# Optimization experiments

Measured on AMD Instinct MI355X. Metric: run time of the kernel, lower is better.

## Reference

```python
import jax, jax.numpy as jnp
import numpy as np

N_HEAD = 16
HEAD_SIZE = 64  # n_embd // n_head = 1024 // 16


def setup_inputs() -> dict:
    key = jax.random.key(0)
    k1, k2 = jax.random.split(key)
    B, T, C = 2, 2048, 1024
    x = jax.random.normal(k1, (B, T, C), dtype=jnp.float32)
    w_attn = jax.random.normal(k2, (C, 3 * C), dtype=jnp.float32) * (C ** -0.5)
    b_attn = jnp.zeros((3 * C,), dtype=jnp.float32)
    return {"x": x, "w_attn": w_attn, "b_attn": b_attn}


def reference(x, w_attn, b_attn):
    B, T, C = x.shape
    qkv = x @ w_attn + b_attn  # [B, T, 3C]
    q, k, v = jnp.split(qkv, 3, axis=-1)
    # [B, T, H, D] -> [B, H, T, D]
    def heads(t):
        return t.reshape(B, T, N_HEAD, HEAD_SIZE).transpose(0, 2, 1, 3)
    q, k, v = heads(q), heads(k), heads(v)
    scale = HEAD_SIZE ** -0.5
    wei = jnp.einsum('bhqd,bhkd->bhqk', q, k) * scale  # [B, H, T, T]
    causal = jnp.tril(jnp.ones((T, T), dtype=bool))
    wei = jnp.where(causal, wei, -jnp.inf)
    wei = jax.nn.softmax(wei, axis=-1)
    out = jnp.einsum('bhqk,bhkd->bhqd', wei, v)  # [B, H, T, D]
    out = out.transpose(0, 2, 1, 3).reshape(B, T, C)
    return out
```

## Files before the change

kernel.cpp:

```cpp
#include <hip/hip_runtime.h>
#include <hip/hip_bf16.h>

#define BSZ 2
#define SEQ 2048
#define CDIM 1024
#define NHEAD 16
#define HDIM 64
#define M_GEMM (BSZ * SEQ)
#define N_GEMM (3 * CDIM)
#define K_GEMM CDIM
#define QK_PITCH (2 * CDIM)

typedef __attribute__((ext_vector_type(8))) short short8;
typedef __attribute__((ext_vector_type(4))) short short4v;
typedef __attribute__((ext_vector_type(4))) float f32x4;

__device__ __forceinline__ short bf16_rn(float f) {
    unsigned u = __builtin_bit_cast(unsigned, f);
    u += 0x7FFF + ((u >> 16) & 1);
    return (short)(u >> 16);
}

__device__ __forceinline__ void gl2lds16(const short* g, short* l) {
    __builtin_amdgcn_global_load_lds(
        (const __attribute__((address_space(1))) unsigned int*)g,
        (__attribute__((address_space(3))) unsigned int*)l, 16, 0, 0);
}

#define WAITV4() asm volatile("s_waitcnt vmcnt(4)")
#define WAITV0() asm volatile("s_waitcnt vmcnt(0)")
#define LGKM0()  asm volatile("s_waitcnt lgkmcnt(0)")
#define SCB()    __builtin_amdgcn_sched_barrier(0)
#define BARRIER() __builtin_amdgcn_s_barrier()

__global__ __launch_bounds__(256) void cvt_fused(const float* __restrict__ X,
                                                 const float* __restrict__ W,
                                                 short* __restrict__ Xb,
                                                 short* __restrict__ WT) {
    const int tid = threadIdx.x;
    if (blockIdx.x < 2048) {
        size_t idx = ((size_t)blockIdx.x * 256 + tid) * 8;
        float4 a = *(const float4*)&X[idx];
        float4 b = *(const float4*)&X[idx + 4];
        short8 o;
        o[0] = bf16_rn(a.x); o[1] = bf16_rn(a.y); o[2] = bf16_rn(a.z); o[3] = bf16_rn(a.w);
        o[4] = bf16_rn(b.x); o[5] = bf16_rn(b.y); o[6] = bf16_rn(b.z); o[7] = bf16_rn(b.w);
        *(short8*)&Xb[idx] = o;
        return;
    }
    __shared__ short T[64][72];
    const int bid = blockIdx.x - 2048;
    const int n0 = (bid % 48) * 64;
    const int k0 = (bid / 48) * 64;
#pragma unroll
    for (int pass = 0; pass < 4; ++pass) {
        int i = pass * 256 + tid;
        int kr = i >> 4;
        int n4 = i & 15;
        float4 v = *(const float4*)&W[(size_t)(k0 + kr) * N_GEMM + n0 + n4 * 4];
        T[n4 * 4 + 0][kr] = bf16_rn(v.x);
        T[n4 * 4 + 1][kr] = bf16_rn(v.y);
        T[n4 * 4 + 2][kr] = bf16_rn(v.z);
        T[n4 * 4 + 3][kr] = bf16_rn(v.w);
    }
    __syncthreads();
#pragma unroll
    for (int pass = 0; pass < 2; ++pass) {
        int o = pass * 256 + tid;
        int nr = o >> 3;
        int c8 = o & 7;
        *(short8*)&WT[(size_t)(n0 + nr) * K_GEMM + k0 + c8 * 8] =
            *(const short8*)&T[nr][c8 * 8];
    }
}

#define MFMA_QUAD(MB, NB)                                                     \
    do {                                                                      \
        __builtin_amdgcn_s_setprio(1);                                        \
        _Pragma("unroll")                                                     \
        for (int mi_ = 0; mi_ < 4; ++mi_)                                     \
            _Pragma("unroll")                                                 \
            for (int ni_ = 0; ni_ < 2; ++ni_)                                 \
                _Pragma("unroll")                                             \
                for (int ks_ = 0; ks_ < 2; ++ks_)                             \
                    acc[(MB) + mi_][(NB) + ni_] =                             \
                        __builtin_amdgcn_mfma_f32_16x16x32_bf16(              \
                            Af[mi_][ks_], Bf[(NB) + ni_][ks_],                \
                            acc[(MB) + mi_][(NB) + ni_], 0, 0, 0);            \
        __builtin_amdgcn_s_setprio(0);                                        \
    } while (0)

__global__ __launch_bounds__(512, 2) void qkv_gemm_8ph(const short* __restrict__ A,
                                                       const short* __restrict__ Bt,
                                                       const float* __restrict__ bias,
                                                       short* __restrict__ Yqk,
                                                       short* __restrict__ Yv) {
    __shared__ short Asl[32768];
    __shared__ short Bsl[32768];

    const int tid  = threadIdx.x;
    const int w    = tid >> 6;
    const int lane = tid & 63;
    const int l16  = lane & 15;
    const int quad = lane >> 4;
    const int wm   = w >> 2;
    const int wn   = w & 3;
    const int ls   = lane >> 3;
    const int lc   = lane & 7;
    const int fsw  = l16 & 7;

    const int orig = blockIdx.y * 12 + blockIdx.x;
    const int xcd  = orig & 7;
    const int idx  = orig >> 3;
    const int bM   = ((xcd & 1) << 3) + (idx & 7);
    const int bN   = (xcd >> 1) * 3 + (idx >> 3);
    const int m0   = bM << 8;
    const int n0   = bN << 8;

    const short* Ab = A  + (size_t)m0 * K_GEMM;
    const short* Bb = Bt + (size_t)n0 * K_GEMM;

    f32x4 acc[8][4];
#pragma unroll
    for (int i = 0; i < 8; ++i)
#pragma unroll
        for (int j = 0; j < 4; ++j) acc[i][j] = (f32x4){0.f, 0.f, 0.f, 0.f};

    auto stageA = [&](int unit, int tt, int sbuf) {
#pragma unroll
        for (int i = 0; i < 2; ++i) {
            const int u0 = (i * 8 + w) * 8;
            const int tr = (u0 & 63) + ((u0 >> 6) << 7) + unit * 64;
            gl2lds16(Ab + (size_t)(tr + ls) * K_GEMM + tt * 64 + ((lc ^ ls) << 3),
                     &Asl[sbuf * 16384 + tr * 64]);
        }
    };
    auto stageB = [&](int unit, int tt, int sbuf) {
#pragma unroll
        for (int i = 0; i < 2; ++i) {
            const int u0 = (i * 8 + w) * 8;
            const int tr = (u0 & 31) + ((u0 >> 5) << 6) + unit * 32;
            gl2lds16(Bb + (size_t)(tr + ls) * K_GEMM + tt * 64 + ((lc ^ ls) << 3),
                     &Bsl[sbuf * 16384 + tr * 64]);
        }
    };
    auto rdA = [&](int ab, int mi, int ks) -> short8 {
        const int r = wm * 128 + mi * 16 + l16;
        return *(const short8*)&Asl[ab + r * 64 + ((ks * 4 + quad) ^ fsw) * 8];
    };
    auto rdB = [&](int ab, int ni, int ks) -> short8 {
        const int r = wn * 64 + ni * 16 + l16;
        return *(const short8*)&Bsl[ab + r * 64 + ((ks * 4 + quad) ^ fsw) * 8];
    };

    stageA(0, 0, 0);
    stageB(0, 0, 0);
    stageB(1, 0, 0);
    stageA(1, 0, 0);
    WAITV4();
    SCB();
    BARRIER();
    SCB();

    for (int t = 0; t < 16; ++t) {
        const int buf = t & 1;
        const int sb  = buf ^ 1;
        const int tn  = (t + 1) & 15;
        const int ab  = buf * 16384;

        short8 Af[4][2], Bf[4][2];

#pragma unroll
        for (int mi = 0; mi < 4; ++mi)
#pragma unroll
            for (int ks = 0; ks < 2; ++ks) Af[mi][ks] = rdA(ab, mi, ks);
#pragma unroll
        for (int ni = 0; ni < 2; ++ni)
#pragma unroll
            for (int ks = 0; ks < 2; ++ks) Bf[ni][ks] = rdB(ab, ni, ks);
        stageA(0, tn, sb);
        SCB(); BARRIER(); LGKM0(); SCB();
        MFMA_QUAD(0, 0);
        WAITV4();
        SCB(); BARRIER(); SCB();

#pragma unroll
        for (int ni = 2; ni < 4; ++ni)
#pragma unroll
            for (int ks = 0; ks < 2; ++ks) Bf[ni][ks] = rdB(ab, ni, ks);
        stageB(0, tn, sb);
        SCB(); BARRIER(); LGKM0(); SCB();
        MFMA_QUAD(0, 2);
        WAITV4();
        SCB(); BARRIER(); SCB();

#pragma unroll
        for (int mi = 0; mi < 4; ++mi)
#pragma unroll
            for (int ks = 0; ks < 2; ++ks) Af[mi][ks] = rdA(ab, 4 + mi, ks);
        stageB(1, tn, sb);
        SCB(); BARRIER(); LGKM0(); SCB();
        MFMA_QUAD(4, 0);
        SCB(); BARRIER(); SCB();

        stageA(1, tn, sb);
        SCB(); BARRIER(); SCB();
        MFMA_QUAD(4, 2);
        WAITV4();
        SCB(); BARRIER(); SCB();
    }
    WAITV0();

    if (n0 >= 2 * CDIM) {
#pragma unroll
        for (int mi = 0; mi < 8; ++mi) {
            int row0 = m0 + wm * 128 + mi * 16 + quad * 4;
#pragma unroll
            for (int ni = 0; ni < 4; ++ni) {
                int colg = n0 + wn * 64 + ni * 16 + l16;
                float bb = bias[colg];
                short4v pk;
#pragma unroll
                for (int r = 0; r < 4; ++r) pk[r] = bf16_rn(acc[mi][ni][r] + bb);
                *(short4v*)&Yv[(size_t)(colg - 2 * CDIM) * M_GEMM + row0] = pk;
            }
        }
    } else {
        const float qs = (n0 < CDIM) ? 0.125f * 1.44269504f : 1.0f;
#pragma unroll
        for (int mi = 0; mi < 8; ++mi)
#pragma unroll
            for (int r = 0; r < 4; ++r) {
                int row = m0 + wm * 128 + mi * 16 + quad * 4 + r;
#pragma unroll
                for (int ni = 0; ni < 4; ++ni) {
                    int colg = n0 + wn * 64 + ni * 16 + l16;
                    Yqk[(size_t)row * QK_PITCH + colg] =
                        bf16_rn((acc[mi][ni][r] + bias[colg]) * qs);
                }
            }
    }
}

__global__ __launch_bounds__(256) void attn_mfma(const short* __restrict__ qk,
                                                 const short* __restrict__ vT,
                                                 float* __restrict__ out) {
    const int b = blockIdx.z;
    const int h = blockIdx.y;
    const int bx = blockIdx.x;
    const int u = h + 16 * b;
    const int band = u >> 3;
    const int base = (band & 2) ? ((bx + 16) & 31) : bx;
    const int qt = (band & 1) ? (31 - base) : base;
    const int tid = threadIdx.x;
    const int w = tid >> 6;
    const int lane = tid & 63;
    const int quad = lane >> 4;
    const int l16 = lane & 15;
    const int q0 = qt * 64;

    __shared__ short Ks[2][64 * 64];
    __shared__ short Vt[2][64 * 64];

    int koff[2], voff[2], ldso[2];
#pragma unroll
    for (int p = 0; p < 2; ++p) {
        int cid = p * 256 + w * 64 + lane;
        int row = cid >> 3;
        int hK = (row & 7) ^ (((row >> 4) & 1) << 2) ^ ((row >> 3) & 1);
        int cK = (cid & 7) ^ hK;
        int cV = (cid & 7) ^ (row & 7);
        koff[p] = row * QK_PITCH + cK * 8;
        voff[p] = row * M_GEMM + cV * 8;
        ldso[p] = (p * 256 + w * 64) * 8;
    }

    const short* qrow = qk + (size_t)(b * SEQ + q0 + w * 16 + l16) * QK_PITCH + h * HDIM;
    short8 aq[2];
    aq[0] = *(const short8*)(qrow + quad * 8);
    aq[1] = *(const short8*)(qrow + 32 + quad * 8);

    float l_run = 0.f;
    f32x4 o_acc[4];
#pragma unroll
    for (int dt = 0; dt < 4; ++dt) o_acc[dt] = (f32x4){0.f, 0.f, 0.f, 0.f};

    const int qglob = q0 + w * 16 + l16;
    const short* kb0 = qk + (size_t)(b * SEQ) * QK_PITCH + CDIM + h * HDIM;
    const short* vb0 = vT + (size_t)(h * HDIM) * M_GEMM + b * SEQ;

    const int ksl = l16 & 7;

    const int Fq = ((l16 >> 2) << 3) + (l16 & 3);

#pragma unroll
    for (int p = 0; p < 2; ++p) {
        gl2lds16(kb0 + koff[p], &Ks[0][ldso[p]]);
        gl2lds16(vb0 + voff[p], &Vt[0][ldso[p]]);
    }
    __syncthreads();

    for (int kt = 0; kt <= qt; ++kt) {
        const int cur = kt & 1;

        if (kt < qt) {
            const short* kbase = kb0 + (size_t)(kt + 1) * 64 * QK_PITCH;
            const short* vbase = vb0 + (kt + 1) * 64;
#pragma unroll
            for (int p = 0; p < 2; ++p) {
                gl2lds16(kbase + koff[p], &Ks[cur ^ 1][ldso[p]]);
                gl2lds16(vbase + voff[p], &Vt[cur ^ 1][ldso[p]]);
            }
        }

        const short* KsC = Ks[cur];
        const short* VtC = Vt[cur];

        f32x4 s[4];
#pragma unroll
        for (int nt = 0; nt < 4; ++nt) s[nt] = (f32x4){0.f, 0.f, 0.f, 0.f};
        __builtin_amdgcn_s_setprio(1);
#pragma unroll
        for (int nt = 0; nt < 4; ++nt) {
            const int F  = (nt >> 1) * 32 + (nt & 1) * 4 + Fq;
            const int hF = (F & 7) ^ (((F >> 4) & 1) << 2) ^ ((F >> 3) & 1);
#pragma unroll
            for (int ks = 0; ks < 2; ++ks) {
                short8 kf = *(const short8*)&KsC[F * 64 + (((ks * 4 + quad) ^ hF) * 8)];
                s[nt] = __builtin_amdgcn_mfma_f32_16x16x32_bf16(kf, aq[ks], s[nt], 0, 0, 0);
            }
        }
        __builtin_amdgcn_s_setprio(0);

        short8 pa0, pa1;
        float lsum = 0.f;
        if (kt < qt) {
#pragma unroll
            for (int nt = 0; nt < 4; ++nt)
#pragma unroll
                for (int r = 0; r < 4; ++r) {
                    float pp = __builtin_amdgcn_exp2f(s[nt][r]);
                    lsum += pp;
                    short pb = bf16_rn(pp);
                    if (nt < 2) pa0[(nt & 1) * 4 + r] = pb;
                    else        pa1[(nt & 1) * 4 + r] = pb;
                }
        } else {
#pragma unroll
            for (int nt = 0; nt < 4; ++nt)
#pragma unroll
                for (int r = 0; r < 4; ++r) {
                    int key = kt * 64 + (nt >> 1) * 32 + quad * 8 + (nt & 1) * 4 + r;
                    float pp = __builtin_amdgcn_exp2f(s[nt][r]);
                    pp = (key > qglob) ? 0.f : pp;
                    lsum += pp;
                    short pb = bf16_rn(pp);
                    if (nt < 2) pa0[(nt & 1) * 4 + r] = pb;
                    else        pa1[(nt & 1) * 4 + r] = pb;
                }
        }
        l_run += lsum;

        __builtin_amdgcn_s_setprio(1);
#pragma unroll
        for (int dt = 0; dt < 4; ++dt)
#pragma unroll
            for (int ks = 0; ks < 2; ++ks) {
                short8 bv = *(const short8*)&VtC[(dt * 16 + l16) * 64 +
                                                 ((ks * 4 + quad) ^ ksl) * 8];
                o_acc[dt] = __builtin_amdgcn_mfma_f32_16x16x32_bf16(
                    ks ? pa1 : pa0, bv, o_acc[dt], 0, 0, 0);
            }
        __builtin_amdgcn_s_setprio(0);

        __syncthreads();
    }

    float l = l_run;
    l += __shfl_xor(l, 16);
    l += __shfl_xor(l, 32);
#pragma unroll
    for (int r = 0; r < 4; ++r) {
        float lq = __shfl(l, quad * 4 + r);
        float inv = 1.f / lq;
        int row = q0 + w * 16 + quad * 4 + r;
        float* optr = out + (size_t)(b * SEQ + row) * CDIM + h * HDIM;
#pragma unroll
        for (int dt = 0; dt < 4; ++dt)
            optr[dt * 16 + l16] = o_acc[dt][r] * inv;
    }
}

extern "C" void kernel_launch(void* const* d_in, const int* in_sizes, int n_in,
                              void* d_out, int out_size, void* d_ws, size_t ws_size,
                              hipStream_t stream) {
    const float* x      = (const float*)d_in[0];
    const float* w_attn = (const float*)d_in[1];
    const float* b_attn = (const float*)d_in[2];
    float* out = (float*)d_out;

    short* qk  = (short*)d_ws;
    short* vT  = (short*)((char*)d_ws + 16777216);
    short* xb  = (short*)((char*)d_ws + 25165824);
    short* wT  = (short*)((char*)d_ws + 33554432);

    cvt_fused<<<2048 + 768, 256, 0, stream>>>(x, w_attn, xb, wT);

    dim3 g1(N_GEMM / 256, M_GEMM / 256);
    qkv_gemm_8ph<<<g1, 512, 0, stream>>>(xb, wT, b_attn, qk, vT);

    dim3 g2(SEQ / 64, NHEAD, BSZ);
    attn_mfma<<<g2, 256, 0, stream>>>(qk, vT, out);
}
```

Baseline: 154.7 us.

## Process two 64-row query tiles per attention block to reuse K/V loads

Each attention workgroup now handles 128 query rows as two 64-row sub-tiles that share the K and V tiles staged in LDS. K fragments are read from LDS once and reused for both QK^T products, and the PV step issues MFMAs for both accumulators against the same V fragment. This halves the grid and roughly halves K/V global and LDS traffic per query. The cost is doubled register use for accumulators, lower occupancy and parallelism, and a simpler block-to-tile order for load balance that reverses the tile index for the second batch. The K swizzle pattern also changes.

```diff
diff --git a/kernel.cpp b/kernel.cpp
--- a/kernel.cpp
+++ b/kernel.cpp
@@ -248,16 +248,15 @@
     const int b = blockIdx.z;
     const int h = blockIdx.y;
     const int bx = blockIdx.x;
-    const int u = h + 16 * b;
-    const int band = u >> 3;
-    const int base = (band & 2) ? ((bx + 16) & 31) : bx;
-    const int qt = (band & 1) ? (31 - base) : base;
+    const int qt = b ? (15 - bx) : bx;
     const int tid = threadIdx.x;
     const int w = tid >> 6;
     const int lane = tid & 63;
     const int quad = lane >> 4;
     const int l16 = lane & 15;
-    const int q0 = qt * 64;
+    const int q0 = qt * 128;
+    const int diag0 = qt * 2;
+    const int ktmax = qt * 2 + 1;
 
     __shared__ short Ks[2][64 * 64];
     __shared__ short Vt[2][64 * 64];
@@ -267,7 +266,7 @@
     for (int p = 0; p < 2; ++p) {
         int cid = p * 256 + w * 64 + lane;
         int row = cid >> 3;
-        int hK = (row & 7) ^ (((row >> 4) & 1) << 2) ^ ((row >> 3) & 1);
+        int hK = (row & 3) | (((row >> 3) & 1) << 2);
         int cK = (cid & 7) ^ hK;
         int cV = (cid & 7) ^ (row & 7);
         koff[p] = row * QK_PITCH + cK * 8;
@@ -275,22 +274,28 @@
         ldso[p] = (p * 256 + w * 64) * 8;
     }
 
-    const short* qrow = qk + (size_t)(b * SEQ + q0 + w * 16 + l16) * QK_PITCH + h * HDIM;
-    short8 aq[2];
-    aq[0] = *(const short8*)(qrow + quad * 8);
-    aq[1] = *(const short8*)(qrow + 32 + quad * 8);
-
-    float l_run = 0.f;
-    f32x4 o_acc[4];
-#pragma unroll
-    for (int dt = 0; dt < 4; ++dt) o_acc[dt] = (f32x4){0.f, 0.f, 0.f, 0.f};
-
-    const int qglob = q0 + w * 16 + l16;
+    const short* q0p = qk + (size_t)(b * SEQ + q0 + w * 16 + l16) * QK_PITCH + h * HDIM;
+    const short* q1p = q0p + (size_t)64 * QK_PITCH;
+    short8 aq0[2], aq1[2];
+    aq0[0] = *(const short8*)(q0p + quad * 8);
+    aq0[1] = *(const short8*)(q0p + 32 + quad * 8);
+    aq1[0] = *(const short8*)(q1p + quad * 8);
+    aq1[1] = *(const short8*)(q1p + 32 + quad * 8);
+
+    float l0 = 0.f, l1 = 0.f;
+    f32x4 o0[4], o1[4];
+#pragma unroll
+    for (int dt = 0; dt < 4; ++dt) {
+        o0[dt] = (f32x4){0.f, 0.f, 0.f, 0.f};
+        o1[dt] = (f32x4){0.f, 0.f, 0.f, 0.f};
+    }
+
+    const int qg0 = q0 + w * 16 + l16;
+    const int qg1 = qg0 + 64;
     const short* kb0 = qk + (size_t)(b * SEQ) * QK_PITCH + CDIM + h * HDIM;
     const short* vb0 = vT + (size_t)(h * HDIM) * M_GEMM + b * SEQ;
 
     const int ksl = l16 & 7;
-
     const int Fq = ((l16 >> 2) << 3) + (l16 & 3);
 
 #pragma unroll
@@ -300,10 +305,10 @@
     }
     __syncthreads();
 
-    for (int kt = 0; kt <= qt; ++kt) {
+    for (int kt = 0; kt <= ktmax; ++kt) {
         const int cur = kt & 1;
 
-        if (kt < qt) {
+        if (kt < ktmax) {
             const short* kbase = kb0 + (size_t)(kt + 1) * 64 * QK_PITCH;
             const short* vbase = vb0 + (kt + 1) * 64;
 #pragma unroll
@@ -315,51 +320,81 @@
 
         const short* KsC = Ks[cur];
         const short* VtC = Vt[cur];
-
-        f32x4 s[4];
-#pragma unroll
-        for (int nt = 0; nt < 4; ++nt) s[nt] = (f32x4){0.f, 0.f, 0.f, 0.f};
-        __builtin_amdgcn_s_setprio(1);
+        const bool run0 = (kt <= diag0);
+
+        short8 kf[4][2];
 #pragma unroll
         for (int nt = 0; nt < 4; ++nt) {
             const int F  = (nt >> 1) * 32 + (nt & 1) * 4 + Fq;
-            const int hF = (F & 7) ^ (((F >> 4) & 1) << 2) ^ ((F >> 3) & 1);
-#pragma unroll
-            for (int ks = 0; ks < 2; ++ks) {
-                short8 kf = *(const short8*)&KsC[F * 64 + (((ks * 4 + quad) ^ hF) * 8)];
-                s[nt] = __builtin_amdgcn_mfma_f32_16x16x32_bf16(kf, aq[ks], s[nt], 0, 0, 0);
-            }
-        }
-        __builtin_amdgcn_s_setprio(0);
-
-        short8 pa0, pa1;
-        float lsum = 0.f;
-        if (kt < qt) {
+            const int hF = (F & 3) | (((F >> 3) & 1) << 2);
+#pragma unroll
+            for (int ks = 0; ks < 2; ++ks)
+                kf[nt][ks] = *(const short8*)&KsC[F * 64 + (((ks * 4 + quad) ^ hF) * 8)];
+        }
+
+        short8 p00, p01;
+        if (run0) {
+            f32x4 s[4];
+#pragma unroll
+            for (int nt = 0; nt < 4; ++nt) s[nt] = (f32x4){0.f, 0.f, 0.f, 0.f};
+            __builtin_amdgcn_s_setprio(1);
+#pragma unroll
+            for (int nt = 0; nt < 4; ++nt)
+#pragma unroll
+                for (int ks = 0; ks < 2; ++ks)
+                    s[nt] = __builtin_amdgcn_mfma_f32_16x16x32_bf16(
+                        kf[nt][ks], aq0[ks], s[nt], 0, 0, 0);
+            __builtin_amdgcn_s_setprio(0);
+            const bool dg = (kt == diag0);
+            float lsum = 0.f;
 #pragma unroll
             for (int nt = 0; nt < 4; ++nt)
 #pragma unroll
                 for (int r = 0; r < 4; ++r) {
                     float pp = __builtin_amdgcn_exp2f(s[nt][r]);
+                    if (dg) {
+                        int key = kt * 64 + (nt >> 1) * 32 + quad * 8 + (nt & 1) * 4 + r;
+                        pp = (key > qg0) ? 0.f : pp;
+                    }
                     lsum += pp;
                     short pb = bf16_rn(pp);
-                    if (nt < 2) pa0[(nt & 1) * 4 + r] = pb;
-                    else        pa1[(nt & 1) * 4 + r] = pb;
+                    if (nt < 2) p00[(nt & 1) * 4 + r] = pb;
+                    else        p01[(nt & 1) * 4 + r] = pb;
                 }
-        } else {
+            l0 += lsum;
+        }
+
+        short8 p10, p11;
+        {
+            f32x4 s[4];
+#pragma unroll
+            for (int nt = 0; nt < 4; ++nt) s[nt] = (f32x4){0.f, 0.f, 0.f, 0.f};
+            __builtin_amdgcn_s_setprio(1);
 #pragma unroll
             for (int nt = 0; nt < 4; ++nt)
 #pragma unroll
+                for (int ks = 0; ks < 2; ++ks)
+                    s[nt] = __builtin_amdgcn_mfma_f32_16x16x32_bf16(
+                        kf[nt][ks], aq1[ks], s[nt], 0, 0, 0);
+            __builtin_amdgcn_s_setprio(0);
+            const bool dg = (kt == ktmax);
+            float lsum = 0.f;
+#pragma unroll
+            for (int nt = 0; nt < 4; ++nt)
+#pragma unroll
                 for (int r = 0; r < 4; ++r) {
-                    int key = kt * 64 + (nt >> 1) * 32 + quad * 8 + (nt & 1) * 4 + r;
                     float pp = __builtin_amdgcn_exp2f(s[nt][r]);
-                    pp = (key > qglob) ? 0.f : pp;
+                    if (dg) {
+                        int key = kt * 64 + (nt >> 1) * 32 + quad * 8 + (nt & 1) * 4 + r;
+                        pp = (key > qg1) ? 0.f : pp;
+                    }
                     lsum += pp;
                     short pb = bf16_rn(pp);
-                    if (nt < 2) pa0[(nt & 1) * 4 + r] = pb;
-                    else        pa1[(nt & 1) * 4 + r] = pb;
+                    if (nt < 2) p10[(nt & 1) * 4 + r] = pb;
+                    else        p11[(nt & 1) * 4 + r] = pb;
                 }
-        }
-        l_run += lsum;
+            l1 += lsum;
+        }
 
         __builtin_amdgcn_s_setprio(1);
 #pragma unroll
@@ -368,26 +403,34 @@
             for (int ks = 0; ks < 2; ++ks) {
                 short8 bv = *(const short8*)&VtC[(dt * 16 + l16) * 64 +
                                                  ((ks * 4 + quad) ^ ksl) * 8];
-                o_acc[dt] = __builtin_amdgcn_mfma_f32_16x16x32_bf16(
-                    ks ? pa1 : pa0, bv, o_acc[dt], 0, 0, 0);
+                if (run0)
+                    o0[dt] = __builtin_amdgcn_mfma_f32_16x16x32_bf16(
+                        ks ? p01 : p00, bv, o0[dt], 0, 0, 0);
+                o1[dt] = __builtin_amdgcn_mfma_f32_16x16x32_bf16(
+                    ks ? p11 : p10, bv, o1[dt], 0, 0, 0);
             }
         __builtin_amdgcn_s_setprio(0);
 
         __syncthreads();
     }
 
-    float l = l_run;
-    l += __shfl_xor(l, 16);
-    l += __shfl_xor(l, 32);
-#pragma unroll
-    for (int r = 0; r < 4; ++r) {
-        float lq = __shfl(l, quad * 4 + r);
-        float inv = 1.f / lq;
-        int row = q0 + w * 16 + quad * 4 + r;
-        float* optr = out + (size_t)(b * SEQ + row) * CDIM + h * HDIM;
-#pragma unroll
-        for (int dt = 0; dt < 4; ++dt)
-            optr[dt * 16 + l16] = o_acc[dt][r] * inv;
+#pragma unroll
+    for (int st = 0; st < 2; ++st) {
+        float l = st ? l1 : l0;
+        l += __shfl_xor(l, 16);
+        l += __shfl_xor(l, 32);
+        const f32x4* o = st ? o1 : o0;
+        const int qb = q0 + st * 64 + w * 16;
+#pragma unroll
+        for (int r = 0; r < 4; ++r) {
+            float lq = __shfl(l, quad * 4 + r);
+            float inv = 1.f / lq;
+            int row = qb + quad * 4 + r;
+            float* optr = out + (size_t)(b * SEQ + row) * CDIM + h * HDIM;
+#pragma unroll
+            for (int dt = 0; dt < 4; ++dt)
+                optr[dt * 16 + l16] = o[dt][r] * inv;
+        }
     }
 }
 
@@ -409,6 +452,6 @@
     dim3 g1(N_GEMM / 256, M_GEMM / 256);
     qkv_gemm_8ph<<<g1, 512, 0, stream>>>(xb, wT, b_attn, qk, vT);
 
-    dim3 g2(SEQ / 64, NHEAD, BSZ);
+    dim3 g2(SEQ / 128, NHEAD, BSZ);
     attn_mfma<<<g2, 256, 0, stream>>>(qk, vT, out);
 }
```

Measured after the change: 177.8 us. 15.0% more time.
